# Kernel optimization log

Measured on AMD Instinct MI355X. Metric: run time of the kernel, lower is better.

Reference implementation:

```python
import jax, jax.numpy as jnp
import numpy as np

CLAMP = 60.0
EPS = 1e-4

def _make_weights(N, alpha_logits, delta_logits, beta_logits):
    alpha = jax.nn.sigmoid(alpha_logits)   # [C,H]
    delta = jax.nn.sigmoid(delta_logits)
    beta = jax.nn.sigmoid(beta_logits)
    A = alpha * beta                        # [C,H]
    r = jnp.clip(1.0 - alpha * delta, EPS, 1.0 - EPS)
    t = jnp.arange(N, dtype=jnp.float32)[:, None, None]   # [N,1,1]
    logr = jnp.clip(jnp.log(r) * t, -CLAMP, CLAMP)        # [N,C,H]
    return A, jnp.exp(logr), jnp.exp(-logr)

def _ema_fwd(x, A, eta, r_pos, r_neg):
    # x: [B,N,C] -> y: [B,N,C]
    z = A * x[..., None] * r_neg            # [B,N,C,H]
    h = jnp.cumsum(z, axis=1) * r_pos       # [B,N,C,H]
    return jnp.sum(eta * h, axis=-1)        # [B,N,C]

def reference(x, alpha_logits, delta_logits, beta_logits, eta, proj_w, proj_b):
    B, N, C = x.shape
    A, r_pos, r_neg = _make_weights(N, alpha_logits, delta_logits, beta_logits)
    xf = x.astype(jnp.float32)
    y_fwd = _ema_fwd(xf, A, eta, r_pos, r_neg)
    y_bwd = _ema_fwd(xf[:, ::-1], A, eta, r_pos, r_neg)[:, ::-1]
    z = jnp.concatenate([y_fwd, y_bwd], axis=-1).astype(x.dtype)  # [B,N,2C]
    return z @ proj_w.T + proj_b            # [B,N,C]

def setup_inputs():
    key = jax.random.key(0)
    ks = jax.random.split(key, 7)
    B, N, C, H = 8, 4096, 512, 4
    return {
        "x": jax.random.normal(ks[0], (B, N, C), dtype=jnp.float32),
        "alpha_logits": jax.random.normal(ks[1], (C, H), dtype=jnp.float32),
        "delta_logits": jax.random.normal(ks[2], (C, H), dtype=jnp.float32),
        "beta_logits": jax.random.normal(ks[3], (C, H), dtype=jnp.float32),
        "eta": jax.random.normal(ks[4], (C, H), dtype=jnp.float32) * 0.02,
        "proj_w": jax.random.normal(ks[5], (C, 2 * C), dtype=jnp.float32) / np.sqrt(2.0 * C),
        "proj_b": jax.random.normal(ks[6], (C,), dtype=jnp.float32) * 0.01,
    }
```

## Files before the change

### kernel.cpp

```cpp
#include <hip/hip_runtime.h>
#include <hip/hip_bf16.h>

#define B_ 8
#define N_ 4096
#define C_ 512
#define H_ 4
#define EPS_ 1e-4f
#define E60P 1.14200739e26f
#define E60M 8.7565108e-27f

typedef __attribute__((ext_vector_type(8))) short short8;
typedef __attribute__((ext_vector_type(4))) float floatx4;
typedef __attribute__((ext_vector_type(2))) float floatx2;
typedef __attribute__((ext_vector_type(4))) unsigned short ushort4_t;
typedef unsigned short ushort_t;

__device__ __forceinline__ float sigmoidf_(float v) {
    return 1.0f / (1.0f + expf(-v));
}

__device__ __forceinline__ int pk_off(int t, int w, int k0, int ks, int f,
                                      int lane8, int kb) {
    return ((((t * 2 + w) * 16 + k0) * 2 + ks) * 4 + f) * 512 + lane8 * 8 + kb;
}

__device__ __forceinline__ void gload16(const void* g, void* l) {
    __builtin_amdgcn_global_load_lds(
        (const __attribute__((address_space(1))) void*)g,
        (__attribute__((address_space(3))) void*)l, 16, 0, 0);
}

__global__ __launch_bounds__(1024, 4) void k_ema_fused(
    const float* __restrict__ x, const float* __restrict__ al,
    const float* __restrict__ dl, const float* __restrict__ bl,
    const float* __restrict__ eta, const float* __restrict__ pw,
    ushort_t* __restrict__ Zp, ushort_t* __restrict__ Wp)
{
    int bid = blockIdx.x;
    int tid = threadIdx.x;

    if (bid >= 256) {
        int i4 = (bid - 256) * 1024 + tid;
        int i  = i4 << 2;
        int n = i >> 10, k = i & 1023;
        int nt = n >> 7, rn = n & 127;
        int k0 = k >> 6, kk = k & 63;
        int off = pk_off(nt, rn >> 6, k0, kk >> 5, (rn >> 4) & 3,
                         ((kk >> 3) & 3) * 16 + (rn & 15), kk & 7);
        float4 v = ((const float4*)pw)[i4];
        ushort4_t r;
        { __hip_bfloat16 t = __float2bfloat16(v.x); r.x = *(ushort_t*)&t; }
        { __hip_bfloat16 t = __float2bfloat16(v.y); r.y = *(ushort_t*)&t; }
        { __hip_bfloat16 t = __float2bfloat16(v.z); r.z = *(ushort_t*)&t; }
        { __hip_bfloat16 t = __float2bfloat16(v.w); r.w = *(ushort_t*)&t; }
        *(ushort4_t*)&Wp[off] = r;
        return;
    }

    __shared__ float slds[32][128];

    int dir  = bid & 1;
    int b    = (bid >> 1) & 7;
    int ct16 = bid >> 4;
    int c5   = tid & 31;
    int sg   = tid >> 5;
    int c    = ct16 * 32 + c5;

    float aa[4], dd[4], bb[4], ee[4];
    { float4 v = ((const float4*)al )[c]; aa[0]=v.x; aa[1]=v.y; aa[2]=v.z; aa[3]=v.w; }
    { float4 v = ((const float4*)dl )[c]; dd[0]=v.x; dd[1]=v.y; dd[2]=v.z; dd[3]=v.w; }
    { float4 v = ((const float4*)bl )[c]; bb[0]=v.x; bb[1]=v.y; bb[2]=v.z; bb[3]=v.w; }
    { float4 v = ((const float4*)eta)[c]; ee[0]=v.x; ee[1]=v.y; ee[2]=v.z; ee[3]=v.w; }

    float A[H_], rr[H_], ri[H_], Lh[H_];
    #pragma unroll
    for (int h = 0; h < H_; ++h) {
        float alpha = sigmoidf_(aa[h]);
        float delta = sigmoidf_(dd[h]);
        float beta  = sigmoidf_(bb[h]);
        A[h] = alpha * beta;
        float r = fminf(fmaxf(1.0f - alpha * delta, EPS_), 1.0f - EPS_);
        Lh[h] = logf(r);
        rr[h] = r;
        ri[h] = 1.0f / r;
    }
    const floatx2 E2M = {E60M, E60M};
    floatx2 ri2[2]  = {{ri[0], ri[1]}, {ri[2], ri[3]}};
    floatx2 rr2[2]  = {{rr[0], rr[1]}, {rr[2], rr[3]}};
    floatx2 ee2[2]  = {{ee[0], ee[1]}, {ee[2], ee[3]}};
    floatx2 AEP2[2] = {{A[0] * E60P, A[1] * E60P}, {A[2] * E60P, A[3] * E60P}};

    int  t0 = sg * 128;
    int  r0 = dir ? (N_ - 1 - t0) : t0;
    long sC = dir ? -(long)C_ : (long)C_;
    const float* xb = x + ((size_t)b * N_ + r0) * C_ + c;

    floatx2 Ae2[2], T2[2];
    #pragma unroll
    for (int p = 0; p < 2; ++p) {
        Ae2[p] = (floatx2){A[2*p]   * expf(fminf(-Lh[2*p]   * (float)t0, 60.0f)),
                           A[2*p+1] * expf(fminf(-Lh[2*p+1] * (float)t0, 60.0f))};
        T2[p]  = (floatx2){0.f, 0.f};
    }
    {
        float cur[8];
        #pragma unroll
        for (int j = 0; j < 8; ++j) cur[j] = xb[(long)j * sC];
        #pragma unroll 1
        for (int g = 0; g < 16; ++g) {
            float nxt[8];
            if (g < 15) {
                #pragma unroll
                for (int j = 0; j < 8; ++j)
                    nxt[j] = xb[(long)(g * 8 + 8 + j) * sC];
            }
            #pragma unroll
            for (int j = 0; j < 8; ++j) {
                floatx2 xv2 = {cur[j], cur[j]};
                #pragma unroll
                for (int p = 0; p < 2; ++p) {
                    T2[p] += Ae2[p] * xv2;
                    Ae2[p] = __builtin_elementwise_min(Ae2[p] * ri2[p], AEP2[p]);
                }
            }
            if (g < 15) {
                #pragma unroll
                for (int j = 0; j < 8; ++j) cur[j] = nxt[j];
            }
        }
    }
    *(float4*)&slds[sg][c5 * 4] = (float4){T2[0].x, T2[0].y, T2[1].x, T2[1].y};

    __syncthreads();

    if (tid < 128) {
        float run = 0.f;
        #pragma unroll
        for (int s = 0; s < 32; ++s) {
            float v = slds[s][tid];
            slds[s][tid] = run;
            run += v;
        }
    }
    __syncthreads();

    floatx2 em2[2], S2[2];
    {
        float4 pf = *(const float4*)&slds[sg][c5 * 4];
        S2[0] = (floatx2){pf.x, pf.y};
        S2[1] = (floatx2){pf.z, pf.w};
    }
    #pragma unroll
    for (int p = 0; p < 2; ++p) {
        Ae2[p] = (floatx2){A[2*p]   * expf(fminf(-Lh[2*p]   * (float)t0, 60.0f)),
                           A[2*p+1] * expf(fminf(-Lh[2*p+1] * (float)t0, 60.0f))};
        em2[p] = (floatx2){expf(fmaxf( Lh[2*p]   * (float)t0, -60.0f)),
                           expf(fmaxf( Lh[2*p+1] * (float)t0, -60.0f))};
    }

    int cl  = (ct16 & 1) * 32 + c5;
    int k0c = (dir ? 8 : 0) + (ct16 >> 1);
    int mtv = b * 32 + (dir ? (31 - sg) : sg);
    int ksv = cl >> 5, qv = (cl >> 3) & 3, kbv = cl & 7;
    int offc0 = pk_off(mtv, 0, k0c, ksv, 0, qv * 16, kbv);
    int offc1 = pk_off(mtv, 1, k0c, ksv, 0, qv * 16, kbv);

    {
        float cur[8];
        #pragma unroll
        for (int j = 0; j < 8; ++j) cur[j] = xb[(long)j * sC];
        #pragma unroll 1
        for (int g = 0; g < 16; ++g) {
            float nxt[8];
            if (g < 15) {
                #pragma unroll
                for (int j = 0; j < 8; ++j)
                    nxt[j] = xb[(long)(g * 8 + 8 + j) * sC];
            }
            #pragma unroll
            for (int j = 0; j < 8; ++j) {
                int jj = g * 8 + j;
                floatx2 xv2 = {cur[j], cur[j]};
                floatx2 acc = {0.f, 0.f};
                #pragma unroll
                for (int p = 0; p < 2; ++p) {
                    S2[p] += Ae2[p] * xv2;
                    Ae2[p] = __builtin_elementwise_min(Ae2[p] * ri2[p], AEP2[p]);
                    acc   += ee2[p] * (em2[p] * S2[p]);
                    em2[p] = __builtin_elementwise_max(em2[p] * rr2[p], E2M);
                }
                float y = acc.x + acc.y;
                __hip_bfloat16 yb = __float2bfloat16(y);
                int q6 = (jj >> 6) & 1;
                int wq = dir ? (1 - q6) : q6;
                int ii = dir ? (63 - (jj & 63)) : (jj & 63);
                int off = (wq ? offc1 : offc0) + ((ii >> 4) << 9) + ((ii & 15) << 3);
                Zp[off] = *(ushort_t*)&yb;
            }
            if (g < 15) {
                #pragma unroll
                for (int j = 0; j < 8; ++j) cur[j] = nxt[j];
            }
        }
    }
}

__global__ __launch_bounds__(256, 4) void k_gemm3(
    const ushort_t* __restrict__ Zp, const ushort_t* __restrict__ Wp,
    const float* __restrict__ bias, float* __restrict__ out)
{
    __shared__ __align__(16) char lds[32768];
    char*  ldsA = lds;
    char*  ldsB = lds + 16384;
    float* stg  = (float*)lds;

    int tid  = threadIdx.x;
    int lane = tid & 63, wave = tid >> 6;
    int wm   = wave & 1, wn = wave >> 1;
    int fr   = lane & 15, quad = lane >> 4;

    int bid = blockIdx.x;
    int mt  = ((bid >> 5) << 3) | (bid & 7);
    int nt  = (bid >> 3) & 3;
    int m0  = mt * 128, n0 = nt * 128;

    const ushort_t* Az = Zp + ((size_t)(mt * 2) * 16) * 4096;
    const ushort_t* Bz = Wp + ((size_t)(nt * 2) * 16) * 4096;

    floatx4 acc[4][4];
    #pragma unroll
    for (int mf = 0; mf < 4; ++mf)
        #pragma unroll
        for (int nf = 0; nf < 4; ++nf)
            acc[mf][nf] = (floatx4){0.f, 0.f, 0.f, 0.f};

    for (int k0 = 0; k0 < 16; ++k0) {
        const ushort_t* As = Az + (size_t)k0 * 4096;
        const ushort_t* Bs = Bz + (size_t)k0 * 4096;
        #pragma unroll
        for (int w = 0; w < 2; ++w)
            #pragma unroll
            for (int inst = 0; inst < 2; ++inst) {
                gload16(As + w * 65536 + inst * 2048 + tid * 8,
                        ldsA + w * 8192 + inst * 4096 + tid * 16);
                gload16(Bs + w * 65536 + inst * 2048 + tid * 8,
                        ldsB + w * 8192 + inst * 4096 + tid * 16);
            }
        asm volatile("s_waitcnt vmcnt(0)" ::: "memory");
        __syncthreads();

        #pragma unroll
        for (int ks = 0; ks < 2; ++ks) {
            short8 af[4], bf[4];
            #pragma unroll
            for (int f = 0; f < 4; ++f) {
                af[f] = *(const short8*)(ldsA + wm * 8192 + (ks * 4 + f) * 1024 + lane * 16);
                bf[f] = *(const short8*)(ldsB + wn * 8192 + (ks * 4 + f) * 1024 + lane * 16);
            }
            #pragma unroll
            for (int mf = 0; mf < 4; ++mf)
                #pragma unroll
                for (int nf = 0; nf < 4; ++nf)
                    acc[mf][nf] = __builtin_amdgcn_mfma_f32_16x16x32_bf16(
                        af[mf], bf[nf], acc[mf][nf], 0, 0, 0);
        }
        __syncthreads();
    }

    int rrow = tid >> 3;
    int seg  = tid & 7;
    int gcol = n0 + seg * 16;

    #pragma unroll
    for (int ch = 0; ch < 4; ++ch) {
        if ((wave & 1) == (ch >> 1)) {
            int ml = (ch & 1) * 2;
            #pragma unroll
            for (int mi = 0; mi < 2; ++mi) {
                #pragma unroll
                for (int nf = 0; nf < 4; ++nf) {
                    int col = wn * 64 + nf * 16 + fr;
                    #pragma unroll
                    for (int rg = 0; rg < 4; ++rg) {
                        int row = mi * 16 + quad * 4 + rg;
                        stg[row * 132 + col] = acc[ml + mi][nf][rg];
                    }
                }
            }
        }
        __syncthreads();
        {
            int gm = m0 + ch * 32 + rrow;
            const float* s = &stg[rrow * 132 + seg * 16];
            #pragma unroll
            for (int k = 0; k < 4; ++k) {
                float4 v  = *(const float4*)&s[k * 4];
                float4 bv = *(const float4*)&bias[gcol + k * 4];
                v.x += bv.x; v.y += bv.y; v.z += bv.z; v.w += bv.w;
                *(float4*)&out[(size_t)gm * 512 + gcol + k * 4] = v;
            }
        }
        __syncthreads();
    }
}

extern "C" void kernel_launch(void* const* d_in, const int* in_sizes, int n_in,
                              void* d_out, int out_size, void* d_ws, size_t ws_size,
                              hipStream_t stream)
{
    const float* x  = (const float*)d_in[0];
    const float* al = (const float*)d_in[1];
    const float* dl = (const float*)d_in[2];
    const float* bl = (const float*)d_in[3];
    const float* et = (const float*)d_in[4];
    const float* pw = (const float*)d_in[5];
    const float* pb = (const float*)d_in[6];
    float* out = (float*)d_out;

    ushort_t* Zp = (ushort_t*)d_ws;
    ushort_t* Wp = (ushort_t*)((char*)d_ws + 67108864);

    hipLaunchKernelGGL(k_ema_fused, dim3(384),  dim3(1024), 0, stream,
                       x, al, dl, bl, et, pw, Zp, Wp);
    hipLaunchKernelGGL(k_gemm3,     dim3(1024), dim3(256),  0, stream,
                       Zp, Wp, pb, out);
}
```

Before: 202.8 us.

## Split EMA scan into 64-step segments over 16 channels with a parallel carry scan

Each EMA block now covers 16 channels and 64 time segments of 64 steps, where it previously covered 32 channels and 32 segments of 128 steps. The grid grows from 256 to 512 scan blocks, and launch bounds ask for 8 blocks per CU. The serial per-thread chain is half as long and there are more blocks to spread across CUs. The cross-segment carry scan now runs on 512 threads, each summing 8 elements followed by a width-8 shuffle scan, instead of a 32-step serial loop on 128 threads. In exchange, each 16-channel row segment loads 64 bytes and makes narrower accesses, and the higher launch bound may force register limits or spills.

```diff
diff --git a/kernel.cpp b/kernel.cpp
--- a/kernel.cpp
+++ b/kernel.cpp
@@ -30,7 +30,7 @@
         (__attribute__((address_space(3))) void*)l, 16, 0, 0);
 }
 
-__global__ __launch_bounds__(1024, 4) void k_ema_fused(
+__global__ __launch_bounds__(1024, 8) void k_ema_fused2(
     const float* __restrict__ x, const float* __restrict__ al,
     const float* __restrict__ dl, const float* __restrict__ bl,
     const float* __restrict__ eta, const float* __restrict__ pw,
@@ -39,8 +39,8 @@
     int bid = blockIdx.x;
     int tid = threadIdx.x;
 
-    if (bid >= 256) {
-        int i4 = (bid - 256) * 1024 + tid;
+    if (bid >= 512) {
+        int i4 = (bid - 512) * 1024 + tid;
         int i  = i4 << 2;
         int n = i >> 10, k = i & 1023;
         int nt = n >> 7, rn = n & 127;
@@ -57,14 +57,14 @@
         return;
     }
 
-    __shared__ float slds[32][128];
-
-    int dir  = bid & 1;
-    int b    = (bid >> 1) & 7;
-    int ct16 = bid >> 4;
-    int c5   = tid & 31;
-    int sg   = tid >> 5;
-    int c    = ct16 * 32 + c5;
+    __shared__ float slds[64][66];
+
+    int dir = bid & 1;
+    int b   = (bid >> 1) & 7;
+    int ct  = bid >> 4;
+    int c4  = tid & 15;
+    int sg  = tid >> 4;
+    int c   = ct * 16 + c4;
 
     float aa[4], dd[4], bb[4], ee[4];
     { float4 v = ((const float4*)al )[c]; aa[0]=v.x; aa[1]=v.y; aa[2]=v.z; aa[3]=v.w; }
@@ -90,7 +90,7 @@
     floatx2 ee2[2]  = {{ee[0], ee[1]}, {ee[2], ee[3]}};
     floatx2 AEP2[2] = {{A[0] * E60P, A[1] * E60P}, {A[2] * E60P, A[3] * E60P}};
 
-    int  t0 = sg * 128;
+    int  t0 = sg * 64;
     int  r0 = dir ? (N_ - 1 - t0) : t0;
     long sC = dir ? -(long)C_ : (long)C_;
     const float* xb = x + ((size_t)b * N_ + r0) * C_ + c;
@@ -107,9 +107,9 @@
         #pragma unroll
         for (int j = 0; j < 8; ++j) cur[j] = xb[(long)j * sC];
         #pragma unroll 1
-        for (int g = 0; g < 16; ++g) {
+        for (int g = 0; g < 8; ++g) {
             float nxt[8];
-            if (g < 15) {
+            if (g < 7) {
                 #pragma unroll
                 for (int j = 0; j < 8; ++j)
                     nxt[j] = xb[(long)(g * 8 + 8 + j) * sC];
@@ -123,33 +123,47 @@
                     Ae2[p] = __builtin_elementwise_min(Ae2[p] * ri2[p], AEP2[p]);
                 }
             }
-            if (g < 15) {
+            if (g < 7) {
                 #pragma unroll
                 for (int j = 0; j < 8; ++j) cur[j] = nxt[j];
             }
         }
     }
-    *(float4*)&slds[sg][c5 * 4] = (float4){T2[0].x, T2[0].y, T2[1].x, T2[1].y};
+    slds[c4 * 4 + 0][sg] = T2[0].x;
+    slds[c4 * 4 + 1][sg] = T2[0].y;
+    slds[c4 * 4 + 2][sg] = T2[1].x;
+    slds[c4 * 4 + 3][sg] = T2[1].y;
 
     __syncthreads();
 
-    if (tid < 128) {
-        float run = 0.f;
-        #pragma unroll
-        for (int s = 0; s < 32; ++s) {
-            float v = slds[s][tid];
-            slds[s][tid] = run;
-            run += v;
+    if (tid < 512) {
+        int seq  = tid >> 3;
+        int slot = tid & 7;
+        float v[8];
+        #pragma unroll
+        for (int j = 0; j < 8; ++j) v[j] = slds[seq][slot * 8 + j];
+        float s = 0.f;
+        #pragma unroll
+        for (int j = 0; j < 8; ++j) s += v[j];
+        float incl = s;
+        #pragma unroll
+        for (int d = 1; d < 8; d <<= 1) {
+            float t = __shfl_up(incl, d, 8);
+            if (slot >= d) incl += t;
+        }
+        float run = incl - s;
+        #pragma unroll
+        for (int j = 0; j < 8; ++j) {
+            float t = v[j];
+            slds[seq][slot * 8 + j] = run;
+            run += t;
         }
     }
     __syncthreads();
 
     floatx2 em2[2], S2[2];
-    {
-        float4 pf = *(const float4*)&slds[sg][c5 * 4];
-        S2[0] = (floatx2){pf.x, pf.y};
-        S2[1] = (floatx2){pf.z, pf.w};
-    }
+    S2[0] = (floatx2){slds[c4 * 4 + 0][sg], slds[c4 * 4 + 1][sg]};
+    S2[1] = (floatx2){slds[c4 * 4 + 2][sg], slds[c4 * 4 + 3][sg]};
     #pragma unroll
     for (int p = 0; p < 2; ++p) {
         Ae2[p] = (floatx2){A[2*p]   * expf(fminf(-Lh[2*p]   * (float)t0, 60.0f)),
@@ -158,21 +172,21 @@
                            expf(fmaxf( Lh[2*p+1] * (float)t0, -60.0f))};
     }
 
-    int cl  = (ct16 & 1) * 32 + c5;
-    int k0c = (dir ? 8 : 0) + (ct16 >> 1);
-    int mtv = b * 32 + (dir ? (31 - sg) : sg);
+    int mt  = b * 32 + (dir ? ((63 - sg) >> 1) : (sg >> 1));
+    int wq  = dir ? ((63 - sg) & 1) : (sg & 1);
+    int k0c = (dir ? 8 : 0) + (ct >> 2);
+    int cl  = (ct & 3) * 16 + c4;
     int ksv = cl >> 5, qv = (cl >> 3) & 3, kbv = cl & 7;
-    int offc0 = pk_off(mtv, 0, k0c, ksv, 0, qv * 16, kbv);
-    int offc1 = pk_off(mtv, 1, k0c, ksv, 0, qv * 16, kbv);
+    int offc = pk_off(mt, wq, k0c, ksv, 0, qv * 16, kbv);
 
     {
         float cur[8];
         #pragma unroll
         for (int j = 0; j < 8; ++j) cur[j] = xb[(long)j * sC];
         #pragma unroll 1
-        for (int g = 0; g < 16; ++g) {
+        for (int g = 0; g < 8; ++g) {
             float nxt[8];
-            if (g < 15) {
+            if (g < 7) {
                 #pragma unroll
                 for (int j = 0; j < 8; ++j)
                     nxt[j] = xb[(long)(g * 8 + 8 + j) * sC];
@@ -191,13 +205,10 @@
                 }
                 float y = acc.x + acc.y;
                 __hip_bfloat16 yb = __float2bfloat16(y);
-                int q6 = (jj >> 6) & 1;
-                int wq = dir ? (1 - q6) : q6;
-                int ii = dir ? (63 - (jj & 63)) : (jj & 63);
-                int off = (wq ? offc1 : offc0) + ((ii >> 4) << 9) + ((ii & 15) << 3);
-                Zp[off] = *(ushort_t*)&yb;
-            }
-            if (g < 15) {
+                int ii = dir ? (63 - jj) : jj;
+                Zp[offc + ((ii >> 4) << 9) + ((ii & 15) << 3)] = *(ushort_t*)&yb;
+            }
+            if (g < 7) {
                 #pragma unroll
                 for (int j = 0; j < 8; ++j) cur[j] = nxt[j];
             }
@@ -320,8 +331,8 @@
     ushort_t* Zp = (ushort_t*)d_ws;
     ushort_t* Wp = (ushort_t*)((char*)d_ws + 67108864);
 
-    hipLaunchKernelGGL(k_ema_fused, dim3(384),  dim3(1024), 0, stream,
+    hipLaunchKernelGGL(k_ema_fused2, dim3(640),  dim3(1024), 0, stream,
                        x, al, dl, bl, et, pw, Zp, Wp);
-    hipLaunchKernelGGL(k_gemm3,     dim3(1024), dim3(256),  0, stream,
+    hipLaunchKernelGGL(k_gemm3,      dim3(1024), dim3(256),  0, stream,
                        Zp, Wp, pb, out);
 }
```

After: 386.1 us. 1.9x slower.

## Double-buffer GEMM LDS stages so global loads overlap MFMA compute

Applied to the files above, without the earlier changes.

The projection GEMM kernel switches from a single-buffered 16-step K loop with 32-wide K chunks to a double-buffered 32-step loop with 16-wide chunks. The next chunk's global-to-LDS loads are issued before the MFMAs on the current buffer, and scheduling barriers keep the two apart. The goal is to hide global memory latency behind matrix compute instead of stalling on each load. The cost is twice as many loop iterations and barriers, and half the MFMA work per sync. It also relies on the packed Zp/Wp layout matching the new half-chunk indexing.

```diff
diff --git a/kernel.cpp b/kernel.cpp
--- a/kernel.cpp
+++ b/kernel.cpp
@@ -205,14 +205,12 @@
     }
 }
 
-__global__ __launch_bounds__(256, 4) void k_gemm3(
+__global__ __launch_bounds__(256, 4) void k_gemm6(
     const ushort_t* __restrict__ Zp, const ushort_t* __restrict__ Wp,
     const float* __restrict__ bias, float* __restrict__ out)
 {
     __shared__ __align__(16) char lds[32768];
-    char*  ldsA = lds;
-    char*  ldsB = lds + 16384;
-    float* stg  = (float*)lds;
+    float* stg = (float*)lds;
 
     int tid  = threadIdx.x;
     int lane = tid & 63, wave = tid >> 6;
@@ -224,8 +222,8 @@
     int nt  = (bid >> 3) & 3;
     int m0  = mt * 128, n0 = nt * 128;
 
-    const ushort_t* Az = Zp + ((size_t)(mt * 2) * 16) * 4096;
-    const ushort_t* Bz = Wp + ((size_t)(nt * 2) * 16) * 4096;
+    const ushort_t* Az = Zp + (size_t)mt * 131072;
+    const ushort_t* Bz = Wp + (size_t)nt * 131072;
 
     floatx4 acc[4][4];
     #pragma unroll
@@ -234,37 +232,45 @@
         for (int nf = 0; nf < 4; ++nf)
             acc[mf][nf] = (floatx4){0.f, 0.f, 0.f, 0.f};
 
-    for (int k0 = 0; k0 < 16; ++k0) {
-        const ushort_t* As = Az + (size_t)k0 * 4096;
-        const ushort_t* Bs = Bz + (size_t)k0 * 4096;
-        #pragma unroll
-        for (int w = 0; w < 2; ++w)
-            #pragma unroll
-            for (int inst = 0; inst < 2; ++inst) {
-                gload16(As + w * 65536 + inst * 2048 + tid * 8,
-                        ldsA + w * 8192 + inst * 4096 + tid * 16);
-                gload16(Bs + w * 65536 + inst * 2048 + tid * 8,
-                        ldsB + w * 8192 + inst * 4096 + tid * 16);
-            }
+    auto STAGE = [&](int bi, int kk) {
+        char* dA = lds + bi * 16384;
+        char* dB = dA + 8192;
+        const ushort_t* As = Az + (size_t)kk * 2048;
+        const ushort_t* Bs = Bz + (size_t)kk * 2048;
+        #pragma unroll
+        for (int w = 0; w < 2; ++w) {
+            gload16(As + w * 65536 + tid * 8, dA + w * 4096 + tid * 16);
+            gload16(Bs + w * 65536 + tid * 8, dB + w * 4096 + tid * 16);
+        }
+    };
+
+    STAGE(0, 0);
+    asm volatile("s_waitcnt vmcnt(0)" ::: "memory");
+    __syncthreads();
+
+    int cur = 0;
+    #pragma unroll 1
+    for (int kk = 0; kk < 32; ++kk) {
+        if (kk < 31) STAGE(cur ^ 1, kk + 1);
+        __builtin_amdgcn_sched_barrier(0);
+        char* ldsA = lds + cur * 16384;
+        char* ldsB = ldsA + 8192;
+        short8 af[4], bf[4];
+        #pragma unroll
+        for (int f = 0; f < 4; ++f) {
+            af[f] = *(const short8*)(ldsA + wm * 4096 + f * 1024 + lane * 16);
+            bf[f] = *(const short8*)(ldsB + wn * 4096 + f * 1024 + lane * 16);
+        }
+        #pragma unroll
+        for (int mf = 0; mf < 4; ++mf)
+            #pragma unroll
+            for (int nf = 0; nf < 4; ++nf)
+                acc[mf][nf] = __builtin_amdgcn_mfma_f32_16x16x32_bf16(
+                    af[mf], bf[nf], acc[mf][nf], 0, 0, 0);
+        __builtin_amdgcn_sched_barrier(0);
         asm volatile("s_waitcnt vmcnt(0)" ::: "memory");
         __syncthreads();
-
-        #pragma unroll
-        for (int ks = 0; ks < 2; ++ks) {
-            short8 af[4], bf[4];
-            #pragma unroll
-            for (int f = 0; f < 4; ++f) {
-                af[f] = *(const short8*)(ldsA + wm * 8192 + (ks * 4 + f) * 1024 + lane * 16);
-                bf[f] = *(const short8*)(ldsB + wn * 8192 + (ks * 4 + f) * 1024 + lane * 16);
-            }
-            #pragma unroll
-            for (int mf = 0; mf < 4; ++mf)
-                #pragma unroll
-                for (int nf = 0; nf < 4; ++nf)
-                    acc[mf][nf] = __builtin_amdgcn_mfma_f32_16x16x32_bf16(
-                        af[mf], bf[nf], acc[mf][nf], 0, 0, 0);
-        }
-        __syncthreads();
+        cur ^= 1;
     }
 
     int rrow = tid >> 3;
@@ -322,6 +328,6 @@
 
     hipLaunchKernelGGL(k_ema_fused, dim3(384),  dim3(1024), 0, stream,
                        x, al, dl, bl, et, pw, Zp, Wp);
-    hipLaunchKernelGGL(k_gemm3,     dim3(1024), dim3(256),  0, stream,
+    hipLaunchKernelGGL(k_gemm6,     dim3(1024), dim3(256),  0, stream,
                        Zp, Wp, pb, out);
 }
```

After: 208.1 us. 2.6% more time.
